# Kernel optimization log

Hardware: AMD Instinct MI355X
Metric: run time of the kernel (lower is better)

## Reference

```python
import jax, jax.numpy as jnp
import numpy as np

HEADS = 16  # config.heads


def setup_inputs() -> dict:
    key = jax.random.key(0)
    k1, k2, k3, k4 = jax.random.split(key, 4)
    B, S, H = 2, 2048, 2048
    x = jax.random.normal(k1, (B, S, H), dtype=jnp.float32)
    w_qkv = jax.random.normal(k2, (H, 3 * H), dtype=jnp.float32) * 0.02
    b_qkv = jax.random.normal(k3, (3 * H,), dtype=jnp.float32) * 0.02
    w_o = jax.random.normal(k4, (H, H), dtype=jnp.float32) * 0.02
    return {"x": x, "w_qkv": w_qkv, "b_qkv": b_qkv, "w_o": w_o}


def reference(x, w_qkv, b_qkv, w_o):
    # pre_layer_norm=False path: plain linear QKV projection
    B, S, H = x.shape
    hd = H // HEADS  # head_size
    scale = 1.0 / jnp.sqrt(jnp.float32(hd))  # 1/norm_factor^2, use_mup=False
    qkv = x @ w_qkv + b_qkv  # [B, S, 3H]
    q, k, v = qkv[..., :H], qkv[..., H:2 * H], qkv[..., 2 * H:]

    def split_heads(t):  # [B,S,H] -> [B,heads,S,hd]
        return t.reshape(B, S, HEADS, hd).transpose(0, 2, 1, 3)

    qh, kh, vh = split_heads(q), split_heads(k), split_heads(v)
    # score_4d_matmul with triangular masking + scale
    scores = jnp.einsum('bhqd,bhkd->bhqk', qh, kh) * scale  # [B,h,S,S]
    causal = jnp.tril(jnp.ones((S, S), dtype=bool))
    scores = jnp.where(causal, scores, -jnp.inf)
    probs = jax.nn.softmax(scores, axis=-1)
    # context_4d_matmul -> merge heads back to [B,S,H]
    ctx = jnp.einsum('bhqk,bhkd->bhqd', probs, vh)
    ctx = ctx.transpose(0, 2, 1, 3).reshape(B, S, H)
    # vector_matmul with attn_ow (no bias in this path)
    out = ctx @ w_o
    return out
```

## Files before the change

kernel.cpp:

```cpp
#include <hip/hip_runtime.h>
#include <cstdint>
#include <cstddef>

typedef __attribute__((ext_vector_type(8))) short bf16x8;
typedef __attribute__((ext_vector_type(4))) float f32x4;
typedef __attribute__((ext_vector_type(4))) unsigned short ushort4_;

#define MFMA16(a, b, c) __builtin_amdgcn_mfma_f32_16x16x32_bf16((a), (b), (c), 0, 0, 0)

__device__ __forceinline__ unsigned short f2bf(float f) {
  union { float f; unsigned u; } c; c.f = f;
  unsigned r = c.u + 0x7fffu + ((c.u >> 16) & 1u);
  return (unsigned short)(r >> 16);
}

__device__ __forceinline__ void gl_lds16(const unsigned short* g, unsigned short* l) {
  __builtin_amdgcn_global_load_lds(
      (const __attribute__((address_space(1))) void*)g,
      (__attribute__((address_space(3))) void*)l, 16, 0, 0);
}

__global__ __launch_bounds__(256) void k_prep(const float* __restrict__ x,
                                              unsigned short* __restrict__ xb,
                                              const float* __restrict__ wqkv,
                                              unsigned short* __restrict__ wqkvT,
                                              const float* __restrict__ wo,
                                              unsigned short* __restrict__ woT) {
  __shared__ unsigned short t[64][65];
  const int blk = blockIdx.x;
  const int tid = threadIdx.x;
  if (blk < 8192) {
    int i = blk * 256 + tid;
    float4 v = reinterpret_cast<const float4*>(x)[i];
    ushort4_ o;
    o.x = f2bf(v.x); o.y = f2bf(v.y); o.z = f2bf(v.z); o.w = f2bf(v.w);
    reinterpret_cast<ushort4_*>(xb)[i] = o;
    return;
  }
  const float* W;
  unsigned short* WT;
  int n0, k0, N;
  if (blk < 11264) {
    int local = blk - 8192;
    W = wqkv; WT = wqkvT; N = 6144;
    n0 = (local % 96) * 64; k0 = (local / 96) * 64;
  } else {
    int local = blk - 11264;
    W = wo; WT = woT; N = 2048;
    n0 = (local % 32) * 64; k0 = (local / 32) * 64;
  }
#pragma unroll
  for (int i = 0; i < 16; i++) {
    int li = tid + i * 256;
    int kk = li >> 6, nn = li & 63;
    t[kk][nn] = f2bf(W[(size_t)(k0 + kk) * N + (n0 + nn)]);
  }
  __syncthreads();
#pragma unroll
  for (int i = 0; i < 16; i++) {
    int li = tid + i * 256;
    int nn = li >> 6, kk = li & 63;
    WT[(size_t)(n0 + nn) * 2048 + (k0 + kk)] = t[kk][nn];
  }
}

template <int MODE>
__global__ __launch_bounds__(256) void k_gemm(const unsigned short* __restrict__ A,
                                              const unsigned short* __restrict__ Bt,
                                              const float* __restrict__ bias,
                                              unsigned short* __restrict__ qb,
                                              unsigned short* __restrict__ kb,
                                              unsigned short* __restrict__ vtb,
                                              float* __restrict__ outp) {
  __shared__ __align__(16) unsigned short As[128 * 64];
  __shared__ __align__(16) unsigned short Bs[128 * 64];
  const int tid = threadIdx.x;
  const int lane = tid & 63, wid = tid >> 6;
  const int quad = lane >> 4, l16 = lane & 15;
  const int wm = wid >> 1, wn = wid & 1;
  const int m0 = blockIdx.y * 128, n0 = blockIdx.x * 128;

  f32x4 acc[4][4];
#pragma unroll
  for (int i = 0; i < 4; i++)
#pragma unroll
    for (int j = 0; j < 4; j++) {
      f32x4 z = {0.f, 0.f, 0.f, 0.f};
      acc[i][j] = z;
    }

  for (int k0 = 0; k0 < 2048; k0 += 64) {
    __syncthreads();
#pragma unroll
    for (int i = 0; i < 4; i++) {
      int slotbase = wid * 64 + i * 256;
      int slot = slotbase + lane;
      int row = slot >> 3, chs = slot & 7, gch = chs ^ (row & 7);
      gl_lds16(A + (size_t)(m0 + row) * 2048 + k0 + gch * 8, &As[slotbase * 8]);
      gl_lds16(Bt + (size_t)(n0 + row) * 2048 + k0 + gch * 8, &Bs[slotbase * 8]);
    }
    __syncthreads();
#pragma unroll
    for (int kc = 0; kc < 2; kc++) {
      bf16x8 af[4], bfr[4];
#pragma unroll
      for (int mt = 0; mt < 4; mt++) {
        int r = wm * 64 + mt * 16 + l16;
        int ch = kc * 4 + quad;
        af[mt] = *reinterpret_cast<const bf16x8*>(&As[r * 64 + ((ch ^ (r & 7)) * 8)]);
      }
#pragma unroll
      for (int nt = 0; nt < 4; nt++) {
        int r = wn * 64 + nt * 16 + l16;
        int ch = kc * 4 + quad;
        bfr[nt] = *reinterpret_cast<const bf16x8*>(&Bs[r * 64 + ((ch ^ (r & 7)) * 8)]);
      }
#pragma unroll
      for (int mt = 0; mt < 4; mt++)
#pragma unroll
        for (int nt = 0; nt < 4; nt++)
          acc[mt][nt] = MFMA16(af[mt], bfr[nt], acc[mt][nt]);
    }
  }

  const int mbase = m0 + wm * 64;
  const int nbase = n0 + wn * 64;
  if (MODE == 0) {
#pragma unroll
    for (int nt = 0; nt < 4; nt++) {
      int n = nbase + nt * 16 + l16;
      float bv = bias[n];
      int seg = n >> 11;
      int h = (n >> 7) & 15;
      int d = n & 127;
#pragma unroll
      for (int mt = 0; mt < 4; mt++) {
        int mrow = mbase + mt * 16 + quad * 4;
        int b = mrow >> 11, s = mrow & 2047;
        if (seg == 2) {
          ushort4_ pk;
          pk.x = f2bf(acc[mt][nt][0] + bv);
          pk.y = f2bf(acc[mt][nt][1] + bv);
          pk.z = f2bf(acc[mt][nt][2] + bv);
          pk.w = f2bf(acc[mt][nt][3] + bv);
          *reinterpret_cast<ushort4_*>(vtb + ((size_t)(b * 16 + h) * 128 + d) * 2048 + s) = pk;
        } else {
          unsigned short* dst = (seg == 0 ? qb : kb);
          size_t base = (size_t)(b * 16 + h) * 2048;
#pragma unroll
          for (int rg = 0; rg < 4; rg++)
            dst[(base + (s + rg)) * 128 + d] = f2bf(acc[mt][nt][rg] + bv);
        }
      }
    }
  } else {
#pragma unroll
    for (int nt = 0; nt < 4; nt++) {
      int n = nbase + nt * 16 + l16;
#pragma unroll
      for (int mt = 0; mt < 4; mt++) {
        int mrow = mbase + mt * 16 + quad * 4;
#pragma unroll
        for (int rg = 0; rg < 4; rg++)
          outp[(size_t)(mrow + rg) * 2048 + n] = acc[mt][nt][rg];
      }
    }
  }
}

__global__ __launch_bounds__(256, 2) void k_attn(const unsigned short* __restrict__ qb,
                                                 const unsigned short* __restrict__ kb,
                                                 const unsigned short* __restrict__ vtb,
                                                 unsigned short* __restrict__ ctx) {
  __shared__ __align__(16) unsigned short Ks[2][64 * 128];
  __shared__ __align__(16) unsigned short Vs[2][128 * 64];
  __shared__ __align__(16) unsigned short Ps[128 * 64];
  const int qt = (gridDim.x - 1) - blockIdx.x;
  const int bh = blockIdx.y;
  const int tid = threadIdx.x;
  const int lane = tid & 63, w = tid >> 6;
  const int quad = lane >> 4, l16 = lane & 15;
  const int qbase = qt * 128;
  const unsigned short* Qh = qb + (size_t)bh * 2048 * 128;
  const unsigned short* Kh = kb + (size_t)bh * 2048 * 128;
  const unsigned short* Vh = vtb + (size_t)bh * 128 * 2048;

  const int q_lo = qbase + w * 32;
  const int nkv = 2 * qt + 2;
  const float sl2 = 0.12751741f;

  bf16x8 qf[2][4];
#pragma unroll
  for (int half = 0; half < 2; half++)
#pragma unroll
    for (int kc = 0; kc < 4; kc++)
      qf[half][kc] = *reinterpret_cast<const bf16x8*>(
          Qh + (size_t)(q_lo + half * 16 + l16) * 128 + kc * 32 + quad * 8);

  f32x4 o[2][8];
#pragma unroll
  for (int half = 0; half < 2; half++)
#pragma unroll
    for (int dt = 0; dt < 8; dt++) {
      f32x4 z = {0.f, 0.f, 0.f, 0.f};
      o[half][dt] = z;
    }
  float m_run[2] = {-1e30f, -1e30f}, l_run[2] = {0.f, 0.f};

  auto stage = [&](int kvb, int bsel) {
    unsigned short* Kd = &Ks[bsel][0];
    unsigned short* Vd = &Vs[bsel][0];
#pragma unroll
    for (int i = 0; i < 4; i++) {
      int slotbase = i * 256 + w * 64;
      int slot = slotbase + lane;
      int rowk = slot >> 4, chk = (slot & 15) ^ (rowk & 7);
      gl_lds16(Kh + (size_t)(kvb + rowk) * 128 + chk * 8, Kd + slotbase * 8);
      int rowv = slot >> 3, chv = (slot & 7) ^ (rowv & 7);
      gl_lds16(Vh + (size_t)rowv * 2048 + kvb + chv * 8, Vd + slotbase * 8);
    }
  };

  stage(0, 0);

  for (int kv = 0; kv < nkv; kv++) {
    const int kvb = kv * 64;
    const int cur = kv & 1;
    asm volatile("s_waitcnt vmcnt(0)" ::: "memory");
    asm volatile("s_barrier" ::: "memory");
    if (kv + 1 < nkv) stage(kvb + 64, cur ^ 1);
    if (kvb > q_lo + 31) continue;

    const unsigned short* Kc = &Ks[cur][0];
    const unsigned short* Vc = &Vs[cur][0];

    f32x4 sacc[2][4];
#pragma unroll
    for (int half = 0; half < 2; half++)
#pragma unroll
      for (int nt = 0; nt < 4; nt++) {
        f32x4 z = {0.f, 0.f, 0.f, 0.f};
        sacc[half][nt] = z;
      }
#pragma unroll
    for (int kc = 0; kc < 4; kc++) {
#pragma unroll
      for (int nt = 0; nt < 4; nt++) {
        int r = nt * 16 + l16, ch = kc * 4 + quad;
        bf16x8 kf = *reinterpret_cast<const bf16x8*>(&Kc[r * 128 + ((ch ^ (r & 7)) * 8)]);
        sacc[0][nt] = MFMA16(kf, qf[0][kc], sacc[0][nt]);
        sacc[1][nt] = MFMA16(kf, qf[1][kc], sacc[1][nt]);
      }
    }

    const bool needmask = (kvb + 63) > q_lo;
#pragma unroll
    for (int half = 0; half < 2; half++) {
      const int qabs = q_lo + half * 16 + l16;
      float tmax = -1e30f;
#pragma unroll
      for (int nt = 0; nt < 4; nt++)
#pragma unroll
        for (int rg = 0; rg < 4; rg++) {
          float v = sacc[half][nt][rg] * sl2;
          if (needmask && (kvb + nt * 16 + quad * 4 + rg) > qabs) v = -1e30f;
          sacc[half][nt][rg] = v;
          tmax = fmaxf(tmax, v);
        }
      tmax = fmaxf(tmax, __shfl_xor(tmax, 16));
      tmax = fmaxf(tmax, __shfl_xor(tmax, 32));
      float mnew = fmaxf(m_run[half], tmax);
      float alpha = exp2f(m_run[half] - mnew);
      m_run[half] = mnew;
      float rsum = 0.f;
#pragma unroll
      for (int nt = 0; nt < 4; nt++)
#pragma unroll
        for (int rg = 0; rg < 4; rg++) {
          float p = exp2f(sacc[half][nt][rg] - mnew);
          sacc[half][nt][rg] = p;
          rsum += p;
        }
      rsum += __shfl_xor(rsum, 16);
      rsum += __shfl_xor(rsum, 32);
      l_run[half] = l_run[half] * alpha + rsum;
#pragma unroll
      for (int dt = 0; dt < 8; dt++)
#pragma unroll
        for (int rg = 0; rg < 4; rg++) o[half][dt][rg] *= alpha;

#pragma unroll
      for (int nt = 0; nt < 4; nt++) {
        ushort4_ pk;
        pk.x = f2bf(sacc[half][nt][0]);
        pk.y = f2bf(sacc[half][nt][1]);
        pk.z = f2bf(sacc[half][nt][2]);
        pk.w = f2bf(sacc[half][nt][3]);
        int chunk = nt * 2 + (quad >> 1);
        *reinterpret_cast<ushort4_*>(
            &Ps[(w * 32 + half * 16 + l16) * 64 + ((chunk ^ (l16 & 7)) * 8) +
                (quad & 1) * 4]) = pk;
      }
    }
    asm volatile("s_waitcnt lgkmcnt(0)" ::: "memory");

#pragma unroll
    for (int kc = 0; kc < 2; kc++) {
      int chunkr = kc * 4 + quad;
      bf16x8 pf0 = *reinterpret_cast<const bf16x8*>(
          &Ps[(w * 32 + l16) * 64 + ((chunkr ^ (l16 & 7)) * 8)]);
      bf16x8 pf1 = *reinterpret_cast<const bf16x8*>(
          &Ps[(w * 32 + 16 + l16) * 64 + ((chunkr ^ (l16 & 7)) * 8)]);
#pragma unroll
      for (int dt = 0; dt < 8; dt++) {
        int r = dt * 16 + l16, ch = kc * 4 + quad;
        bf16x8 vf = *reinterpret_cast<const bf16x8*>(&Vc[r * 64 + ((ch ^ (r & 7)) * 8)]);
        o[0][dt] = MFMA16(vf, pf0, o[0][dt]);
        o[1][dt] = MFMA16(vf, pf1, o[1][dt]);
      }
    }
  }

  const int b = bh >> 4, h = bh & 15;
#pragma unroll
  for (int half = 0; half < 2; half++) {
    const float inv = 1.f / l_run[half];
    const int s = q_lo + half * 16 + l16;
#pragma unroll
    for (int dt = 0; dt < 8; dt++) {
      int d0 = dt * 16 + quad * 4;
      ushort4_ pk;
      pk.x = f2bf(o[half][dt][0] * inv);
      pk.y = f2bf(o[half][dt][1] * inv);
      pk.z = f2bf(o[half][dt][2] * inv);
      pk.w = f2bf(o[half][dt][3] * inv);
      *reinterpret_cast<ushort4_*>(
          &ctx[((size_t)b * 2048 + s) * 2048 + h * 128 + d0]) = pk;
    }
  }
}

extern "C" void kernel_launch(void* const* d_in, const int* in_sizes, int n_in,
                              void* d_out, int out_size, void* d_ws, size_t ws_size,
                              hipStream_t stream) {
  const float* x = (const float*)d_in[0];
  const float* w_qkv = (const float*)d_in[1];
  const float* b_qkv = (const float*)d_in[2];
  const float* w_o = (const float*)d_in[3];
  float* outp = (float*)d_out;

  unsigned short* ws = (unsigned short*)d_ws;
  unsigned short* xb    = ws;
  unsigned short* wqkvT = xb + 8388608;
  unsigned short* woT   = wqkvT + 12582912;
  unsigned short* qbuf  = woT + 4194304;
  unsigned short* kbuf  = qbuf + 8388608;
  unsigned short* vtbuf = kbuf + 8388608;
  unsigned short* ctxb  = vtbuf + 8388608;

  k_prep<<<12288, 256, 0, stream>>>(x, xb, w_qkv, wqkvT, w_o, woT);
  k_gemm<0><<<dim3(48, 32), 256, 0, stream>>>(xb, wqkvT, b_qkv, qbuf, kbuf, vtbuf, nullptr);
  k_attn<<<dim3(16, 32), 256, 0, stream>>>(qbuf, kbuf, vtbuf, ctxb);
  k_gemm<1><<<dim3(16, 32), 256, 0, stream>>>(ctxb, woT, nullptr, nullptr, nullptr, nullptr, outp);
}
```

Before: 423.3 us.

## Pair causal query tiles per block, fold scale into Q, lazy softmax rescale

The attention kernel now gives each block two 64-row query strips taken from opposite ends of the sequence (j and 31-j). This evens out causal work across blocks. KV tiles beyond the short strip's diagonal run only the long strip's MFMAs. The softmax scale is folded into Q in the QKV GEMM epilogue, which removes a per-score multiply. The online-softmax rescale of O and l is skipped unless the running max grows by more than 8 in log2 units. That skip saves vector work but lets unnormalized probabilities reach about 256 before they are converted to bf16.

```diff
diff --git a/kernel.cpp b/kernel.cpp
--- a/kernel.cpp
+++ b/kernel.cpp
@@ -133,6 +133,7 @@
       int seg = n >> 11;
       int h = (n >> 7) & 15;
       int d = n & 127;
+      float sc = (seg == 0) ? 0.12751741f : 1.0f;
 #pragma unroll
       for (int mt = 0; mt < 4; mt++) {
         int mrow = mbase + mt * 16 + quad * 4;
@@ -149,7 +150,7 @@
           size_t base = (size_t)(b * 16 + h) * 2048;
 #pragma unroll
           for (int rg = 0; rg < 4; rg++)
-            dst[(base + (s + rg)) * 128 + d] = f2bf(acc[mt][nt][rg] + bv);
+            dst[(base + (s + rg)) * 128 + d] = f2bf((acc[mt][nt][rg] + bv) * sc);
         }
       }
     }
@@ -175,27 +176,27 @@
   __shared__ __align__(16) unsigned short Ks[2][64 * 128];
   __shared__ __align__(16) unsigned short Vs[2][128 * 64];
   __shared__ __align__(16) unsigned short Ps[128 * 64];
-  const int qt = (gridDim.x - 1) - blockIdx.x;
+  const int j = blockIdx.x;
   const int bh = blockIdx.y;
   const int tid = threadIdx.x;
   const int lane = tid & 63, w = tid >> 6;
   const int quad = lane >> 4, l16 = lane & 15;
-  const int qbase = qt * 128;
   const unsigned short* Qh = qb + (size_t)bh * 2048 * 128;
   const unsigned short* Kh = kb + (size_t)bh * 2048 * 128;
   const unsigned short* Vh = vtb + (size_t)bh * 128 * 2048;
 
-  const int q_lo = qbase + w * 32;
-  const int nkv = 2 * qt + 2;
-  const float sl2 = 0.12751741f;
+  const int base0 = j * 64 + w * 16;
+  const int base1 = (31 - j) * 64 + w * 16;
+  const int nkv = 32 - j;
 
   bf16x8 qf[2][4];
 #pragma unroll
-  for (int half = 0; half < 2; half++)
-#pragma unroll
-    for (int kc = 0; kc < 4; kc++)
-      qf[half][kc] = *reinterpret_cast<const bf16x8*>(
-          Qh + (size_t)(q_lo + half * 16 + l16) * 128 + kc * 32 + quad * 8);
+  for (int kc = 0; kc < 4; kc++) {
+    qf[0][kc] = *reinterpret_cast<const bf16x8*>(
+        Qh + (size_t)(base0 + l16) * 128 + kc * 32 + quad * 8);
+    qf[1][kc] = *reinterpret_cast<const bf16x8*>(
+        Qh + (size_t)(base1 + l16) * 128 + kc * 32 + quad * 8);
+  }
 
   f32x4 o[2][8];
 #pragma unroll
@@ -221,6 +222,58 @@
     }
   };
 
+  auto softmax_half = [&](f32x4 (&sa)[4], f32x4 (&oo)[8], float& mr, float& lr,
+                          int qb_h, int psrow, int kvb) {
+    const bool needmask = (kvb + 63) > qb_h;
+    const int qabs = qb_h + l16;
+    float tmax = -1e30f;
+#pragma unroll
+    for (int nt = 0; nt < 4; nt++)
+#pragma unroll
+      for (int rg = 0; rg < 4; rg++) {
+        float v = sa[nt][rg];
+        if (needmask && (kvb + nt * 16 + quad * 4 + rg) > qabs) v = -1e30f;
+        sa[nt][rg] = v;
+        tmax = fmaxf(tmax, v);
+      }
+    tmax = fmaxf(tmax, __shfl_xor(tmax, 16));
+    tmax = fmaxf(tmax, __shfl_xor(tmax, 32));
+    if (!__all(tmax - mr <= 8.f)) {
+      float mnew = fmaxf(mr, tmax);
+      float alpha = exp2f(mr - mnew);
+      mr = mnew;
+      lr *= alpha;
+#pragma unroll
+      for (int dt = 0; dt < 8; dt++)
+#pragma unroll
+        for (int rg = 0; rg < 4; rg++) oo[dt][rg] *= alpha;
+    }
+    const float mcur = mr;
+    float rsum = 0.f;
+#pragma unroll
+    for (int nt = 0; nt < 4; nt++)
+#pragma unroll
+      for (int rg = 0; rg < 4; rg++) {
+        float p = exp2f(sa[nt][rg] - mcur);
+        sa[nt][rg] = p;
+        rsum += p;
+      }
+    rsum += __shfl_xor(rsum, 16);
+    rsum += __shfl_xor(rsum, 32);
+    lr += rsum;
+#pragma unroll
+    for (int nt = 0; nt < 4; nt++) {
+      ushort4_ pk;
+      pk.x = f2bf(sa[nt][0]);
+      pk.y = f2bf(sa[nt][1]);
+      pk.z = f2bf(sa[nt][2]);
+      pk.w = f2bf(sa[nt][3]);
+      int chunk = nt * 2 + (quad >> 1);
+      *reinterpret_cast<ushort4_*>(
+          &Ps[(psrow + l16) * 64 + ((chunk ^ (l16 & 7)) * 8) + (quad & 1) * 4]) = pk;
+    }
+  };
+
   stage(0, 0);
 
   for (int kv = 0; kv < nkv; kv++) {
@@ -229,7 +282,7 @@
     asm volatile("s_waitcnt vmcnt(0)" ::: "memory");
     asm volatile("s_barrier" ::: "memory");
     if (kv + 1 < nkv) stage(kvb + 64, cur ^ 1);
-    if (kvb > q_lo + 31) continue;
+    const bool dual = (kv <= j);
 
     const unsigned short* Kc = &Ks[cur][0];
     const unsigned short* Vc = &Vs[cur][0];
@@ -242,81 +295,59 @@
         f32x4 z = {0.f, 0.f, 0.f, 0.f};
         sacc[half][nt] = z;
       }
-#pragma unroll
-    for (int kc = 0; kc < 4; kc++) {
-#pragma unroll
-      for (int nt = 0; nt < 4; nt++) {
-        int r = nt * 16 + l16, ch = kc * 4 + quad;
-        bf16x8 kf = *reinterpret_cast<const bf16x8*>(&Kc[r * 128 + ((ch ^ (r & 7)) * 8)]);
-        sacc[0][nt] = MFMA16(kf, qf[0][kc], sacc[0][nt]);
-        sacc[1][nt] = MFMA16(kf, qf[1][kc], sacc[1][nt]);
-      }
-    }
-
-    const bool needmask = (kvb + 63) > q_lo;
-#pragma unroll
-    for (int half = 0; half < 2; half++) {
-      const int qabs = q_lo + half * 16 + l16;
-      float tmax = -1e30f;
-#pragma unroll
-      for (int nt = 0; nt < 4; nt++)
-#pragma unroll
-        for (int rg = 0; rg < 4; rg++) {
-          float v = sacc[half][nt][rg] * sl2;
-          if (needmask && (kvb + nt * 16 + quad * 4 + rg) > qabs) v = -1e30f;
-          sacc[half][nt][rg] = v;
-          tmax = fmaxf(tmax, v);
-        }
-      tmax = fmaxf(tmax, __shfl_xor(tmax, 16));
-      tmax = fmaxf(tmax, __shfl_xor(tmax, 32));
-      float mnew = fmaxf(m_run[half], tmax);
-      float alpha = exp2f(m_run[half] - mnew);
-      m_run[half] = mnew;
-      float rsum = 0.f;
-#pragma unroll
-      for (int nt = 0; nt < 4; nt++)
-#pragma unroll
-        for (int rg = 0; rg < 4; rg++) {
-          float p = exp2f(sacc[half][nt][rg] - mnew);
-          sacc[half][nt][rg] = p;
-          rsum += p;
-        }
-      rsum += __shfl_xor(rsum, 16);
-      rsum += __shfl_xor(rsum, 32);
-      l_run[half] = l_run[half] * alpha + rsum;
-#pragma unroll
-      for (int dt = 0; dt < 8; dt++)
-#pragma unroll
-        for (int rg = 0; rg < 4; rg++) o[half][dt][rg] *= alpha;
-
-#pragma unroll
-      for (int nt = 0; nt < 4; nt++) {
-        ushort4_ pk;
-        pk.x = f2bf(sacc[half][nt][0]);
-        pk.y = f2bf(sacc[half][nt][1]);
-        pk.z = f2bf(sacc[half][nt][2]);
-        pk.w = f2bf(sacc[half][nt][3]);
-        int chunk = nt * 2 + (quad >> 1);
-        *reinterpret_cast<ushort4_*>(
-            &Ps[(w * 32 + half * 16 + l16) * 64 + ((chunk ^ (l16 & 7)) * 8) +
-                (quad & 1) * 4]) = pk;
-      }
-    }
+    if (dual) {
+#pragma unroll
+      for (int kc = 0; kc < 4; kc++)
+#pragma unroll
+        for (int nt = 0; nt < 4; nt++) {
+          int r = nt * 16 + l16, ch = kc * 4 + quad;
+          bf16x8 kf = *reinterpret_cast<const bf16x8*>(&Kc[r * 128 + ((ch ^ (r & 7)) * 8)]);
+          sacc[0][nt] = MFMA16(kf, qf[0][kc], sacc[0][nt]);
+          sacc[1][nt] = MFMA16(kf, qf[1][kc], sacc[1][nt]);
+        }
+    } else {
+#pragma unroll
+      for (int kc = 0; kc < 4; kc++)
+#pragma unroll
+        for (int nt = 0; nt < 4; nt++) {
+          int r = nt * 16 + l16, ch = kc * 4 + quad;
+          bf16x8 kf = *reinterpret_cast<const bf16x8*>(&Kc[r * 128 + ((ch ^ (r & 7)) * 8)]);
+          sacc[1][nt] = MFMA16(kf, qf[1][kc], sacc[1][nt]);
+        }
+    }
+
+    softmax_half(sacc[1], o[1], m_run[1], l_run[1], base1, w * 32 + 16, kvb);
+    if (dual) softmax_half(sacc[0], o[0], m_run[0], l_run[0], base0, w * 32, kvb);
     asm volatile("s_waitcnt lgkmcnt(0)" ::: "memory");
 
-#pragma unroll
-    for (int kc = 0; kc < 2; kc++) {
-      int chunkr = kc * 4 + quad;
-      bf16x8 pf0 = *reinterpret_cast<const bf16x8*>(
-          &Ps[(w * 32 + l16) * 64 + ((chunkr ^ (l16 & 7)) * 8)]);
-      bf16x8 pf1 = *reinterpret_cast<const bf16x8*>(
-          &Ps[(w * 32 + 16 + l16) * 64 + ((chunkr ^ (l16 & 7)) * 8)]);
-#pragma unroll
-      for (int dt = 0; dt < 8; dt++) {
-        int r = dt * 16 + l16, ch = kc * 4 + quad;
-        bf16x8 vf = *reinterpret_cast<const bf16x8*>(&Vc[r * 64 + ((ch ^ (r & 7)) * 8)]);
-        o[0][dt] = MFMA16(vf, pf0, o[0][dt]);
-        o[1][dt] = MFMA16(vf, pf1, o[1][dt]);
+    if (dual) {
+#pragma unroll
+      for (int kc = 0; kc < 2; kc++) {
+        int chunkr = kc * 4 + quad;
+        bf16x8 pf0 = *reinterpret_cast<const bf16x8*>(
+            &Ps[(w * 32 + l16) * 64 + ((chunkr ^ (l16 & 7)) * 8)]);
+        bf16x8 pf1 = *reinterpret_cast<const bf16x8*>(
+            &Ps[(w * 32 + 16 + l16) * 64 + ((chunkr ^ (l16 & 7)) * 8)]);
+#pragma unroll
+        for (int dt = 0; dt < 8; dt++) {
+          int r = dt * 16 + l16, ch = kc * 4 + quad;
+          bf16x8 vf = *reinterpret_cast<const bf16x8*>(&Vc[r * 64 + ((ch ^ (r & 7)) * 8)]);
+          o[0][dt] = MFMA16(vf, pf0, o[0][dt]);
+          o[1][dt] = MFMA16(vf, pf1, o[1][dt]);
+        }
+      }
+    } else {
+#pragma unroll
+      for (int kc = 0; kc < 2; kc++) {
+        int chunkr = kc * 4 + quad;
+        bf16x8 pf1 = *reinterpret_cast<const bf16x8*>(
+            &Ps[(w * 32 + 16 + l16) * 64 + ((chunkr ^ (l16 & 7)) * 8)]);
+#pragma unroll
+        for (int dt = 0; dt < 8; dt++) {
+          int r = dt * 16 + l16, ch = kc * 4 + quad;
+          bf16x8 vf = *reinterpret_cast<const bf16x8*>(&Vc[r * 64 + ((ch ^ (r & 7)) * 8)]);
+          o[1][dt] = MFMA16(vf, pf1, o[1][dt]);
+        }
       }
     }
   }
@@ -325,7 +356,7 @@
 #pragma unroll
   for (int half = 0; half < 2; half++) {
     const float inv = 1.f / l_run[half];
-    const int s = q_lo + half * 16 + l16;
+    const int s = (half == 0 ? base0 : base1) + l16;
 #pragma unroll
     for (int dt = 0; dt < 8; dt++) {
       int d0 = dt * 16 + quad * 4;
```

New measurement: 399.4 us. 1.06x faster.
